# Kernel tuning notes

Measured on AMD Instinct MI355X. Metric: run time of the kernel, lower is better.

## Reference

```python
import jax, jax.numpy as jnp
import numpy as np

B, N, D, H, IN, HID = 16, 1024, 256, 8, 256, 1024
HD = IN // H  # head dim = 32
EPS = 1e-5


def layer_norm(x, g, b):
    mu = jnp.mean(x, axis=-1, keepdims=True)
    var = jnp.var(x, axis=-1, keepdims=True)
    return (x - mu) / jnp.sqrt(var + EPS) * g + b


def setup_inputs() -> dict:
    key = jax.random.key(0)
    ks = jax.random.split(key, 12)
    s = 0.02
    return {
        "x": jax.random.normal(ks[0], (B, N, D), jnp.float32),
        "coords": jax.random.normal(ks[1], (B, N, 2), jnp.float32),
        "g1": jnp.ones((D,), jnp.float32),
        "b1": jnp.zeros((D,), jnp.float32),
        "Wqkv": jax.random.normal(ks[2], (3 * IN, D), jnp.float32) * s,
        "Wproj": jax.random.normal(ks[3], (IN, IN), jnp.float32) * s,
        "bproj": jnp.zeros((IN,), jnp.float32),
        "g2": jnp.ones((D,), jnp.float32),
        "b2": jnp.zeros((D,), jnp.float32),
        "W1": jax.random.normal(ks[4], (HID, D), jnp.float32) * s,
        "bb1": jnp.zeros((HID,), jnp.float32),
        "W2": jax.random.normal(ks[5], (D, HID), jnp.float32) * s,
        "bb2": jnp.zeros((D,), jnp.float32),
    }


def reference(x, coords, g1, b1, Wqkv, Wproj, bproj, g2, b2, W1, bb1, W2, bb2):
    # ---- Attention branch (pre-norm) ----
    h = layer_norm(x, g1, b1)                       # [B,N,D]
    qkv = h @ Wqkv.T                                # [B,N,3*IN]
    qkv = qkv.reshape(B, N, 3, H, HD).transpose(2, 0, 3, 1, 4)  # [3,B,H,N,HD]
    q, k, v = qkv[0], qkv[1], qkv[2]
    scale = HD ** -0.5
    attn = jnp.einsum('bhid,bhjd->bhij', q * scale, k)  # [B,H,N,N]
    attn = jax.nn.softmax(attn, axis=-1)
    o = jnp.einsum('bhij,bhjd->bhid', attn, v)      # [B,H,N,HD]
    o = o.transpose(0, 2, 1, 3).reshape(B, N, IN)   # [B,N,IN]
    o = o @ Wproj.T + bproj
    o = o + h                                       # residual inside Attention (vs normed input)
    x = x + o                                       # Block residual (double residual, faithful)
    # ---- MLP branch ----
    h2 = layer_norm(x, g2, b2)
    m = jax.nn.gelu(h2 @ W1.T + bb1, approximate=False) @ W2.T + bb2
    return x + m
```

## Files before the change

kernel.cpp:

```cpp
#include <hip/hip_runtime.h>
#include <hip/hip_bf16.h>
#include <math.h>

#define Bdim 16
#define Ndim 1024
#define Ddim 256
#define Hdim 8
#define HDdim 32
#define INdim 256
#define HIDdim 1024
#define Tdim (Bdim * Ndim)

typedef __attribute__((ext_vector_type(8)))  short bf16x8;
typedef __attribute__((ext_vector_type(4)))  short bf16x4;
typedef __attribute__((ext_vector_type(16))) float f32x16;
typedef unsigned int u32;

__device__ inline short f2bf(float x) {
    union { __hip_bfloat16 b; short s; } u;
    u.b = __float2bfloat16(x);
    return u.s;
}

__device__ inline float bf2f(short s) {
    return __uint_as_float(((u32)(unsigned short)s) << 16);
}

__device__ inline float fexp2(float x) {
#if __has_builtin(__builtin_amdgcn_exp2f)
    return __builtin_amdgcn_exp2f(x);
#else
    return exp2f(x);
#endif
}

__device__ inline u32 pack2bf(float a, float b) {
#if __has_builtin(__builtin_amdgcn_cvt_pk_bf16_f32)
    typedef __attribute__((ext_vector_type(2))) __bf16 bf16x2_t;
    union { bf16x2_t v; u32 u; } c;
    c.v = __builtin_amdgcn_cvt_pk_bf16_f32(a, b);
    return c.u;
#else
    u32 ua = __float_as_uint(a), ub = __float_as_uint(b);
    return ((ua + 0x8000u) >> 16) | ((ub + 0x8000u) & 0xffff0000u);
#endif
}

__device__ inline void plswap(u32 &a, u32 &b) {
    asm volatile("v_permlane32_swap_b32 %0, %1" : "+v"(a), "+v"(b));
}

__device__ inline float gelu_exact(float v) {
    return 0.5f * v * (1.0f + erff(v * 0.70710678118654752f));
}

#define N4_QKV  (3 * INdim * Ddim / 4)
#define N4_PROJ (INdim * INdim / 4)
#define N4_W1   (HIDdim * Ddim / 4)
#define N4_W2   (Ddim * HIDdim / 4)

__global__ __launch_bounds__(256) void cvt_all_kernel(const float* __restrict__ s0,
                                                      const float* __restrict__ s1,
                                                      const float* __restrict__ s2,
                                                      const float* __restrict__ s3,
                                                      short* __restrict__ d0,
                                                      short* __restrict__ d1,
                                                      short* __restrict__ d2,
                                                      short* __restrict__ d3) {
    int i = blockIdx.x * 256 + threadIdx.x;
    const float* src; short* dst; int j;
    if (i < N4_QKV)                          { src = s0; dst = d0; j = i; }
    else if (i < N4_QKV + N4_PROJ)           { src = s1; dst = d1; j = i - N4_QKV; }
    else if (i < N4_QKV + N4_PROJ + N4_W1)   { src = s2; dst = d2; j = i - N4_QKV - N4_PROJ; }
    else                                     { src = s3; dst = d3; j = i - N4_QKV - N4_PROJ - N4_W1; }
    float4 v = ((const float4*)src)[j];
    bf16x4 b;
    b[0] = f2bf(v.x); b[1] = f2bf(v.y); b[2] = f2bf(v.z); b[3] = f2bf(v.w);
    ((bf16x4*)dst)[j] = b;
}

__global__ __launch_bounds__(256) void ln4_kernel(const float* __restrict__ x,
                                                  const float* __restrict__ g,
                                                  const float* __restrict__ b,
                                                  float* __restrict__ outf,
                                                  short* __restrict__ outb) {
    int w = threadIdx.x >> 6, lane = threadIdx.x & 63;
    int row = blockIdx.x * 4 + w;
    float4 v = ((const float4*)x)[(size_t)row * 64 + lane];
    float s  = (v.x + v.y) + (v.z + v.w);
    float s2 = (v.x * v.x + v.y * v.y) + (v.z * v.z + v.w * v.w);
    #pragma unroll
    for (int off = 32; off; off >>= 1) {
        s  += __shfl_xor(s,  off, 64);
        s2 += __shfl_xor(s2, off, 64);
    }
    float mu   = s * (1.0f / Ddim);
    float var  = s2 * (1.0f / Ddim) - mu * mu;
    float rstd = rsqrtf(var + 1e-5f);
    float4 gg = ((const float4*)g)[lane];
    float4 bb = ((const float4*)b)[lane];
    float4 r;
    r.x = (v.x - mu) * rstd * gg.x + bb.x;
    r.y = (v.y - mu) * rstd * gg.y + bb.y;
    r.z = (v.z - mu) * rstd * gg.z + bb.z;
    r.w = (v.w - mu) * rstd * gg.w + bb.w;
    if (outf) ((float4*)outf)[(size_t)row * 64 + lane] = r;
    bf16x4 rb;
    rb[0] = f2bf(r.x); rb[1] = f2bf(r.y); rb[2] = f2bf(r.z); rb[3] = f2bf(r.w);
    ((bf16x4*)outb)[(size_t)row * 64 + lane] = rb;
}

#define EPI_NONE 0
#define EPI_PROJ 1
#define EPI_GELU 2
#define EPI_RES  3
#define EPI_QKV  4

#define GPAD64 72
#define SCALE2Q 0.25505654249892417f

template <int EPI, int BN>
__global__ __launch_bounds__(256) void gemm_mfma(const short* __restrict__ A,
                                                 const short* __restrict__ W,
                                                 void* __restrict__ Cv,
                                                 int M, int N, int K,
                                                 const float* __restrict__ bias,
                                                 const float* __restrict__ add1,
                                                 const float* __restrict__ add2) {
    __shared__ short As[128 * GPAD64];
    __shared__ short Bs[BN * GPAD64];
    const int tid = threadIdx.x, w = tid >> 6, lane = tid & 63;
    const int col = lane & 31;
    const int half_id = lane >> 5;
    const int m0 = blockIdx.y * 128, n0 = blockIdx.x * BN;
    const int wm = (BN == 128) ? (w & 1) * 64 : w * 32;
    const int wn = (BN == 128) ? (w >> 1) * 64 : 0;
    constexpr int TM = (BN == 128) ? 2 : 1;

    f32x16 acc[TM][2];
    #pragma unroll
    for (int i = 0; i < TM; ++i) { acc[i][0] = 0.0f; acc[i][1] = 0.0f; }

    const int sra = tid >> 1, ssa = (tid & 1) * 32;
    const int srb = (BN == 128) ? (tid >> 1) : (tid >> 2);
    const int ssb = (BN == 128) ? (tid & 1) * 32 : (tid & 3) * 16;
    constexpr int NB = (BN == 128) ? 4 : 2;

    const short* pAsrc = &A[(size_t)(m0 + sra) * K + ssa];
    const short* pBsrc = &W[(size_t)(n0 + srb) * K + ssb];

    bf16x8 pa[4], pb[NB];
    #pragma unroll
    for (int j = 0; j < 4; ++j) pa[j] = *(const bf16x8*)&pAsrc[j * 8];
    #pragma unroll
    for (int j = 0; j < NB; ++j) pb[j] = *(const bf16x8*)&pBsrc[j * 8];

    const int T = K >> 6;
    for (int kt = 0; kt < T; ++kt) {
        __syncthreads();
        #pragma unroll
        for (int j = 0; j < 4; ++j) *(bf16x8*)&As[sra * GPAD64 + ssa + j * 8] = pa[j];
        #pragma unroll
        for (int j = 0; j < NB; ++j) *(bf16x8*)&Bs[srb * GPAD64 + ssb + j * 8] = pb[j];
        __syncthreads();

        if (kt + 1 < T) {
            const short* a = pAsrc + (kt + 1) * 64;
            const short* b = pBsrc + (kt + 1) * 64;
            #pragma unroll
            for (int j = 0; j < 4; ++j) pa[j] = *(const bf16x8*)&a[j * 8];
            #pragma unroll
            for (int j = 0; j < NB; ++j) pb[j] = *(const bf16x8*)&b[j * 8];
        }

        #pragma unroll
        for (int ks = 0; ks < 4; ++ks) {
            bf16x8 af[TM], bfv[2];
            #pragma unroll
            for (int t = 0; t < TM; ++t)
                af[t] = *(const bf16x8*)&As[(wm + t * 32 + col) * GPAD64 + ks * 16 + half_id * 8];
            #pragma unroll
            for (int t = 0; t < 2; ++t)
                bfv[t] = *(const bf16x8*)&Bs[(wn + t * 32 + col) * GPAD64 + ks * 16 + half_id * 8];
            #pragma unroll
            for (int tm = 0; tm < TM; ++tm)
                #pragma unroll
                for (int tn = 0; tn < 2; ++tn)
                    acc[tm][tn] = __builtin_amdgcn_mfma_f32_32x32x16_bf16(
                        af[tm], bfv[tn], acc[tm][tn], 0, 0, 0);
        }
    }

    float* Cf = (float*)Cv;
    short* Cb = (short*)Cv;
    #pragma unroll
    for (int tm = 0; tm < TM; ++tm) {
        #pragma unroll
        for (int r = 0; r < 16; ++r) {
            int row = m0 + wm + tm * 32 + (r & 3) + 8 * (r >> 2) + 4 * half_id;
            #pragma unroll
            for (int tn = 0; tn < 2; ++tn) {
                int cn = n0 + wn + tn * 32 + col;
                size_t off = (size_t)row * N + cn;
                float v = acc[tm][tn][r];
                if (EPI != EPI_NONE && EPI != EPI_QKV) v += bias[cn];
                if (EPI == EPI_QKV && cn < 256) v *= SCALE2Q;
                if (EPI == EPI_GELU) v = gelu_exact(v);
                if (EPI == EPI_PROJ) v += add1[off] + add2[off];
                if (EPI == EPI_RES)  v += add1[off];
                if (EPI == EPI_PROJ || EPI == EPI_RES) Cf[off] = v;
                else                                   Cb[off] = f2bf(v);
            }
        }
    }
}

#define VTPAD 136

__global__ __launch_bounds__(256) void vtrans_kernel(const short* __restrict__ qkv,
                                                     short* __restrict__ vT) {
    __shared__ short Tl[32 * VTPAD];
    const int tid = threadIdx.x;
    const int bh = blockIdx.x, c = blockIdx.y;
    const int b = bh >> 3, head = bh & 7;
    {
        int r = tid >> 1, hv = tid & 1;
        const short* src = qkv + (size_t)b * Ndim * 768 + (size_t)(c * 128 + r) * 768
                           + 512 + head * 32 + hv * 16;
        bf16x8 v0 = *(const bf16x8*)&src[0];
        bf16x8 v1 = *(const bf16x8*)&src[8];
        #pragma unroll
        for (int i = 0; i < 8; ++i) {
            Tl[(hv * 16 + i) * VTPAD + r]     = v0[i];
            Tl[(hv * 16 + 8 + i) * VTPAD + r] = v1[i];
        }
    }
    __syncthreads();
    {
        int d = tid >> 3, j16 = (tid & 7) * 16;
        short* dst = vT + (size_t)(bh * 32 + d) * Ndim + c * 128 + j16;
        *(bf16x8*)&dst[0] = *(const bf16x8*)&Tl[d * VTPAD + j16];
        *(bf16x8*)&dst[8] = *(const bf16x8*)&Tl[d * VTPAD + j16 + 8];
    }
}

#define KVPAD 40
#define CHUNK 128

__global__ __launch_bounds__(256) void attn_mfma_kernel(const short* __restrict__ qkv,
                                                        const short* __restrict__ vT,
                                                        short* __restrict__ opart,
                                                        float* __restrict__ lpart) {
    __shared__ short Ks[CHUNK * KVPAD];
    __shared__ short Vt[32 * VTPAD];

    const int tid = threadIdx.x;
    const int w = tid >> 6;
    const int lane = tid & 63;
    const int col = lane & 31;
    const int half_id = lane >> 5;

    const int bh = blockIdx.y;
    const int b = bh >> 3, head = bh & 7;
    const int q0w = blockIdx.x * 128 + w * 32;
    const int part = blockIdx.z;

    const size_t qkvb = (size_t)b * Ndim * 768;
    short* op = opart + (size_t)part * Tdim * 256;
    float* lp = lpart + (size_t)part * Tdim * 8;

    bf16x8 qf[2];
    {
        const short* qrow = qkv + qkvb + (size_t)(q0w + col) * 768 + head * 32;
        #pragma unroll
        for (int kh = 0; kh < 2; ++kh)
            qf[kh] = *(const bf16x8*)&qrow[kh * 16 + half_id * 8];
    }

    bf16x8 vone;
    #pragma unroll
    for (int i = 0; i < 8; ++i) vone[i] = (short)0x3F80;

    f32x16 o_acc = 0.0f, l_acc = 0.0f;

    const int c0 = part * 4;
    for (int c = c0; c < c0 + 4; ++c) {
        if (c != c0) __syncthreads();
        {
            int r = tid >> 1, hv = tid & 1;
            const short* src = qkv + qkvb + (size_t)(c * CHUNK + r) * 768
                               + head * 32 + hv * 16;
            *(bf16x8*)&Ks[r * KVPAD + hv * 16]     = *(const bf16x8*)&src[256];
            *(bf16x8*)&Ks[r * KVPAD + hv * 16 + 8] = *(const bf16x8*)&src[256 + 8];
            int d = tid >> 3, j16 = (tid & 7) * 16;
            const short* vsrc = vT + (size_t)(bh * 32 + d) * Ndim + c * CHUNK + j16;
            *(bf16x8*)&Vt[d * VTPAD + j16]     = *(const bf16x8*)&vsrc[0];
            *(bf16x8*)&Vt[d * VTPAD + j16 + 8] = *(const bf16x8*)&vsrc[8];
        }
        __syncthreads();

        #pragma unroll
        for (int jt = 0; jt < 4; ++jt) {
            bf16x8 kf0 = *(bf16x8*)&Ks[(jt * 32 + col) * KVPAD + half_id * 8];
            bf16x8 kf1 = *(bf16x8*)&Ks[(jt * 32 + col) * KVPAD + 16 + half_id * 8];
            bf16x8 vf0 = *(bf16x8*)&Vt[col * VTPAD + jt * 32 + half_id * 8];
            bf16x8 vf1 = *(bf16x8*)&Vt[col * VTPAD + jt * 32 + 16 + half_id * 8];

            f32x16 s_acc = 0.0f;
            s_acc = __builtin_amdgcn_mfma_f32_32x32x16_bf16(kf0, qf[0], s_acc, 0, 0, 0);
            s_acc = __builtin_amdgcn_mfma_f32_32x32x16_bf16(kf1, qf[1], s_acc, 0, 0, 0);

            u32 wd[8];
            #pragma unroll
            for (int g = 0; g < 8; ++g) {
                float e0 = fexp2(s_acc[2 * g + 0]);
                float e1 = fexp2(s_acc[2 * g + 1]);
                wd[g] = pack2bf(e0, e1);
            }
            plswap(wd[0], wd[2]); plswap(wd[1], wd[3]);
            plswap(wd[4], wd[6]); plswap(wd[5], wd[7]);

            union { u32 u[4]; bf16x8 v; } p0, p1;
            p0.u[0] = wd[0]; p0.u[1] = wd[1]; p0.u[2] = wd[2]; p0.u[3] = wd[3];
            p1.u[0] = wd[4]; p1.u[1] = wd[5]; p1.u[2] = wd[6]; p1.u[3] = wd[7];

            __builtin_amdgcn_s_setprio(1);
            o_acc = __builtin_amdgcn_mfma_f32_32x32x16_bf16(p0.v, vf0, o_acc, 0, 0, 0);
            o_acc = __builtin_amdgcn_mfma_f32_32x32x16_bf16(p1.v, vf1, o_acc, 0, 0, 0);
            l_acc = __builtin_amdgcn_mfma_f32_32x32x16_bf16(p0.v, vone, l_acc, 0, 0, 0);
            l_acc = __builtin_amdgcn_mfma_f32_32x32x16_bf16(p1.v, vone, l_acc, 0, 0, 0);
            __builtin_amdgcn_s_setprio(0);
        }
    }

    #pragma unroll
    for (int r = 0; r < 16; ++r) {
        int q_r = (r & 3) + 8 * (r >> 2) + 4 * half_id;
        size_t gq = (size_t)(b * Ndim + q0w + q_r);
        op[gq * INdim + head * 32 + col] = f2bf(o_acc[r]);
    }
    if (col < 16) {
        int r = col;
        int q_r = (r & 3) + 8 * (r >> 2) + 4 * half_id;
        lp[(size_t)(b * Ndim + q0w + q_r) * 8 + head] = l_acc[r];
    }
}

__global__ __launch_bounds__(256) void combine_kernel(const short* __restrict__ opart,
                                                      const float* __restrict__ lpart,
                                                      short* __restrict__ oat) {
    int i = blockIdx.x * 256 + threadIdx.x;
    size_t base = (size_t)i * 8;
    int gq = (int)(base >> 8);
    int head = ((int)(base & 255)) >> 5;
    bf16x8 a = ((const bf16x8*)opart)[i];
    bf16x8 b = ((const bf16x8*)(opart + (size_t)Tdim * 256))[i];
    float l = lpart[(size_t)gq * 8 + head] + lpart[(size_t)Tdim * 8 + (size_t)gq * 8 + head];
    float rl = 1.0f / l;
    bf16x8 r;
    #pragma unroll
    for (int j = 0; j < 8; ++j) r[j] = f2bf((bf2f(a[j]) + bf2f(b[j])) * rl);
    ((bf16x8*)oat)[i] = r;
}

extern "C" void kernel_launch(void* const* d_in, const int* in_sizes, int n_in,
                              void* d_out, int out_size, void* d_ws, size_t ws_size,
                              hipStream_t stream) {
    const float* x     = (const float*)d_in[0];
    const float* g1    = (const float*)d_in[2];
    const float* b1    = (const float*)d_in[3];
    const float* Wqkv  = (const float*)d_in[4];
    const float* Wproj = (const float*)d_in[5];
    const float* bproj = (const float*)d_in[6];
    const float* g2    = (const float*)d_in[7];
    const float* b2    = (const float*)d_in[8];
    const float* W1    = (const float*)d_in[9];
    const float* bb1   = (const float*)d_in[10];
    const float* W2    = (const float*)d_in[11];
    const float* bb2   = (const float*)d_in[12];
    float* out = (float*)d_out;

    char* ws = (char*)d_ws;
    float* h      = (float*)(ws);
    short* h_bf   = (short*)(ws + (size_t)(16u << 20));
    short* qkv_bf = (short*)(ws + (size_t)(24u << 20));
    float* xnew   = (float*)(ws + (size_t)(24u << 20));
    short* oat_bf = (short*)(ws + (size_t)(40u << 20));
    short* opart  = (short*)(ws + (size_t)(48u << 20));
    short* mid_bf = (short*)(ws + (size_t)(48u << 20));
    float* lpart  = (float*)(ws + (size_t)(80u << 20));
    short* vT     = (short*)(ws + (size_t)(81u << 20));
    short* wqkv_b = (short*)(ws + (size_t)(89u << 20));
    short* wproj_b= (short*)(ws + (size_t)(89u << 20) + 768 * 1024);
    short* w1_b   = (short*)(ws + (size_t)(90u << 20));
    short* w2_b   = (short*)(ws + (size_t)(90u << 20) + 512 * 1024);

    cvt_all_kernel<<<(N4_QKV + N4_PROJ + N4_W1 + N4_W2 + 255) / 256, 256, 0, stream>>>(
        Wqkv, Wproj, W1, W2, wqkv_b, wproj_b, w1_b, w2_b);

    ln4_kernel<<<Tdim / 4, 256, 0, stream>>>(x, g1, b1, h, h_bf);
    gemm_mfma<EPI_QKV, 128><<<dim3(768 / 128, Tdim / 128), 256, 0, stream>>>(
        h_bf, wqkv_b, qkv_bf, Tdim, 768, 256, nullptr, nullptr, nullptr);
    vtrans_kernel<<<dim3(Bdim * Hdim, Ndim / 128), 256, 0, stream>>>(qkv_bf, vT);
    attn_mfma_kernel<<<dim3(Ndim / 128, Bdim * Hdim, 2), 256, 0, stream>>>(
        qkv_bf, vT, opart, lpart);
    combine_kernel<<<(Tdim * INdim / 8) / 256, 256, 0, stream>>>(opart, lpart, oat_bf);
    gemm_mfma<EPI_PROJ, 64><<<dim3(256 / 64, Tdim / 128), 256, 0, stream>>>(
        oat_bf, wproj_b, xnew, Tdim, 256, 256, bproj, h, x);
    ln4_kernel<<<Tdim / 4, 256, 0, stream>>>(xnew, g2, b2, nullptr, h_bf);
    gemm_mfma<EPI_GELU, 128><<<dim3(1024 / 128, Tdim / 128), 256, 0, stream>>>(
        h_bf, w1_b, mid_bf, Tdim, 1024, 256, bb1, nullptr, nullptr);
    gemm_mfma<EPI_RES, 64><<<dim3(256 / 64, Tdim / 128), 256, 0, stream>>>(
        mid_bf, w2_b, out, Tdim, 256, 1024, bb2, xnew, nullptr);
}
```

Measured before the change: 222.0 us.

## Prefetch next KV chunk into registers and software-pipeline QK MFMAs with softmax

Loads the next K/V chunk from global memory into registers while the current chunk is being computed, so global latency overlaps with MFMA work instead of sitting between barriers. Inside each chunk, the QK^T score tile for the next 32-key subtile is computed before the exp/PV work on the current one, so the exp instructions can overlap with independent MFMAs. The cost is higher register pressure from the extra s_next accumulator and the prefetch registers, which could lower occupancy.

```diff
diff --git a/kernel.cpp b/kernel.cpp
--- a/kernel.cpp
+++ b/kernel.cpp
@@ -269,6 +269,11 @@
     short* op = opart + (size_t)part * Tdim * 256;
     float* lp = lpart + (size_t)part * Tdim * 8;
 
+    const int sr = tid >> 1, shv = tid & 1;
+    const short* ksrc = qkv + qkvb + (size_t)sr * 768 + 256 + head * 32 + shv * 16;
+    const int sd = tid >> 3, sj16 = (tid & 7) * 16;
+    const short* vsrc = vT + (size_t)(bh * 32 + sd) * Ndim + sj16;
+
     bf16x8 qf[2];
     {
         const short* qrow = qkv + qkvb + (size_t)(q0w + col) * 768 + head * 32;
@@ -284,37 +289,64 @@
     f32x16 o_acc = 0.0f, l_acc = 0.0f;
 
     const int c0 = part * 4;
-    for (int c = c0; c < c0 + 4; ++c) {
-        if (c != c0) __syncthreads();
+
+    bf16x8 rk0, rk1, rv0, rv1;
+    {
+        const short* kp = ksrc + (size_t)(c0 * CHUNK) * 768;
+        rk0 = *(const bf16x8*)&kp[0];
+        rk1 = *(const bf16x8*)&kp[8];
+        const short* vp = vsrc + c0 * CHUNK;
+        rv0 = *(const bf16x8*)&vp[0];
+        rv1 = *(const bf16x8*)&vp[8];
+    }
+
+    #pragma unroll
+    for (int ci = 0; ci < 4; ++ci) {
+        if (ci != 0) __syncthreads();
+        *(bf16x8*)&Ks[sr * KVPAD + shv * 16]     = rk0;
+        *(bf16x8*)&Ks[sr * KVPAD + shv * 16 + 8] = rk1;
+        *(bf16x8*)&Vt[sd * VTPAD + sj16]     = rv0;
+        *(bf16x8*)&Vt[sd * VTPAD + sj16 + 8] = rv1;
+        __syncthreads();
+
+        if (ci < 3) {
+            const short* kp = ksrc + (size_t)((c0 + ci + 1) * CHUNK) * 768;
+            rk0 = *(const bf16x8*)&kp[0];
+            rk1 = *(const bf16x8*)&kp[8];
+            const short* vp = vsrc + (c0 + ci + 1) * CHUNK;
+            rv0 = *(const bf16x8*)&vp[0];
+            rv1 = *(const bf16x8*)&vp[8];
+        }
+
+        f32x16 s_cur;
         {
-            int r = tid >> 1, hv = tid & 1;
-            const short* src = qkv + qkvb + (size_t)(c * CHUNK + r) * 768
-                               + head * 32 + hv * 16;
-            *(bf16x8*)&Ks[r * KVPAD + hv * 16]     = *(const bf16x8*)&src[256];
-            *(bf16x8*)&Ks[r * KVPAD + hv * 16 + 8] = *(const bf16x8*)&src[256 + 8];
-            int d = tid >> 3, j16 = (tid & 7) * 16;
-            const short* vsrc = vT + (size_t)(bh * 32 + d) * Ndim + c * CHUNK + j16;
-            *(bf16x8*)&Vt[d * VTPAD + j16]     = *(const bf16x8*)&vsrc[0];
-            *(bf16x8*)&Vt[d * VTPAD + j16 + 8] = *(const bf16x8*)&vsrc[8];
-        }
-        __syncthreads();
-
+            bf16x8 kf0 = *(bf16x8*)&Ks[col * KVPAD + half_id * 8];
+            bf16x8 kf1 = *(bf16x8*)&Ks[col * KVPAD + 16 + half_id * 8];
+            f32x16 z = 0.0f;
+            z = __builtin_amdgcn_mfma_f32_32x32x16_bf16(kf0, qf[0], z, 0, 0, 0);
+            z = __builtin_amdgcn_mfma_f32_32x32x16_bf16(kf1, qf[1], z, 0, 0, 0);
+            s_cur = z;
+        }
         #pragma unroll
         for (int jt = 0; jt < 4; ++jt) {
-            bf16x8 kf0 = *(bf16x8*)&Ks[(jt * 32 + col) * KVPAD + half_id * 8];
-            bf16x8 kf1 = *(bf16x8*)&Ks[(jt * 32 + col) * KVPAD + 16 + half_id * 8];
+            f32x16 s_next;
+            if (jt < 3) {
+                bf16x8 kf0 = *(bf16x8*)&Ks[((jt + 1) * 32 + col) * KVPAD + half_id * 8];
+                bf16x8 kf1 = *(bf16x8*)&Ks[((jt + 1) * 32 + col) * KVPAD + 16 + half_id * 8];
+                f32x16 z = 0.0f;
+                z = __builtin_amdgcn_mfma_f32_32x32x16_bf16(kf0, qf[0], z, 0, 0, 0);
+                z = __builtin_amdgcn_mfma_f32_32x32x16_bf16(kf1, qf[1], z, 0, 0, 0);
+                s_next = z;
+            }
+
             bf16x8 vf0 = *(bf16x8*)&Vt[col * VTPAD + jt * 32 + half_id * 8];
             bf16x8 vf1 = *(bf16x8*)&Vt[col * VTPAD + jt * 32 + 16 + half_id * 8];
 
-            f32x16 s_acc = 0.0f;
-            s_acc = __builtin_amdgcn_mfma_f32_32x32x16_bf16(kf0, qf[0], s_acc, 0, 0, 0);
-            s_acc = __builtin_amdgcn_mfma_f32_32x32x16_bf16(kf1, qf[1], s_acc, 0, 0, 0);
-
             u32 wd[8];
             #pragma unroll
             for (int g = 0; g < 8; ++g) {
-                float e0 = fexp2(s_acc[2 * g + 0]);
-                float e1 = fexp2(s_acc[2 * g + 1]);
+                float e0 = fexp2(s_cur[2 * g + 0]);
+                float e1 = fexp2(s_cur[2 * g + 1]);
                 wd[g] = pack2bf(e0, e1);
             }
             plswap(wd[0], wd[2]); plswap(wd[1], wd[3]);
@@ -330,6 +362,8 @@
             l_acc = __builtin_amdgcn_mfma_f32_32x32x16_bf16(p0.v, vone, l_acc, 0, 0, 0);
             l_acc = __builtin_amdgcn_mfma_f32_32x32x16_bf16(p1.v, vone, l_acc, 0, 0, 0);
             __builtin_amdgcn_s_setprio(0);
+
+            if (jt < 3) s_cur = s_next;
         }
     }
 
```

Result: no change. 219.8 us (-1.0%).
